# Kernel tuning notes

Measured on AMD Instinct MI355X. Metric: run time of the kernel, lower is better.

## Reference

```python
import jax, jax.numpy as jnp
import numpy as np

B, S, D, H, E, K = 16, 2048, 768, 3072, 8, 2
CAP_FACTOR = 1.25
LN_EPS = 1e-5


def setup_inputs() -> dict:
    key = jax.random.key(0)
    ks = jax.random.split(key, 6)
    scale = 0.02
    return {
        "x": jax.random.normal(ks[0], (B, S, D), jnp.float32),
        "w_gate": jax.random.normal(ks[1], (D, E), jnp.float32) * scale,  # router (eval: no noise)
        "w1": jax.random.normal(ks[2], (E, D, H), jnp.float32) * scale,
        "b1": jnp.zeros((E, H), jnp.float32),
        "w2": jax.random.normal(ks[3], (E, H, D), jnp.float32) * scale,
        "b2": jnp.zeros((E, D), jnp.float32),
        "ln_w": jnp.ones((D,), jnp.float32),
        "ln_b": jnp.zeros((D,), jnp.float32),
    }


def reference(x, w_gate, w1, b1, w2, b2, ln_w, ln_b):
    b, s, d = x.shape
    n = b * s
    capacity = int(CAP_FACTOR * n * K / E)  # static, matches _compute_capacity
    xf = x.reshape(n, d)

    # NoisyTopKRouter in eval mode: linear gate -> top-k -> softmax over top-k logits
    logits = xf @ w_gate                                   # [N, E]
    top_logits, top_idx = jax.lax.top_k(logits, K)         # [N, K]
    routing = jax.nn.softmax(top_logits, axis=-1)          # [N, K]

    out = jnp.zeros((n, d), x.dtype)
    for e in range(E):
        # per-token weight for expert e (0 if not routed to e)
        w_e = jnp.sum(routing * (top_idx == e), axis=-1)   # [N]
        # capacity dropping: keep the `capacity` highest-weight tokens.
        # Unassigned tokens have weight 0 -> zero contribution, so selecting
        # them as filler is mathematically identical to the torch loop.
        top_w, tok = jax.lax.top_k(w_e, capacity)          # [cap], [cap]
        sel = xf[tok]                                      # gather [cap, D]
        h = jax.nn.gelu(sel @ w1[e] + b1[e], approximate=False)
        y = h @ w2[e] + b2[e]                              # [cap, D]
        out = out.at[tok].add(y * top_w[:, None])          # weighted scatter-add

    out = out.reshape(b, s, d)
    mu = jnp.mean(out, axis=-1, keepdims=True)
    var = jnp.mean(jnp.square(out - mu), axis=-1, keepdims=True)
    return (out - mu) * jax.lax.rsqrt(var + LN_EPS) * ln_w + ln_b
```

## Files before the change

### kernel.cpp

```cpp
#include <hip/hip_runtime.h>
#include <math.h>

#define NTOK 32768
#define DDIM 768
#define HDIM 3072
#define NEXP 8
#define CAP  10240

typedef short short8 __attribute__((ext_vector_type(8)));
typedef float f32x4 __attribute__((ext_vector_type(4)));

__device__ __forceinline__ unsigned short f2bf(float f) {
  unsigned u = __float_as_uint(f);
  u += 0x7FFFu + ((u >> 16) & 1u);
  return (unsigned short)(u >> 16);
}
__device__ __forceinline__ float bf2f(unsigned short h) {
  return __uint_as_float((unsigned)h << 16);
}

__device__ __forceinline__ void gload16(const void* g, void* l) {
  __builtin_amdgcn_global_load_lds(
      (const __attribute__((address_space(1))) void*)g,
      (__attribute__((address_space(3))) void*)l, 16, 0, 0);
}

__device__ __forceinline__ float gelu_fast(float v) {
  float z = v * 0.70710678118654752f;
  float a = fabsf(z);
  float t = 1.0f / (1.0f + 0.3275911f * a);
  float p = t * (0.254829592f +
           t * (-0.284496736f +
           t * (1.421413741f +
           t * (-1.453152027f +
           t * 1.061405429f))));
  float ex = __expf(-a * a);
  float er = 1.0f - p * ex;
  er = copysignf(er, z);
  return 0.5f * v * (1.0f + er);
}

__global__ __launch_bounds__(256) void router_assign(
    const float* __restrict__ x, const float* __restrict__ wg,
    unsigned short* __restrict__ xb,
    unsigned int* __restrict__ pair, float* __restrict__ pw)
{
  __shared__ float wt[NEXP][DDIM];
  int t = threadIdx.x;
  for (int idx = t; idx < NEXP * DDIM; idx += 256) {
    int d = idx >> 3, e = idx & 7;
    wt[e][d] = wg[idx];
  }
  __syncthreads();
  int wave = t >> 6, lane = t & 63;
  int n0 = blockIdx.x * 32 + wave * 8;
  for (int i = 0; i < 8; ++i) {
    int n = n0 + i;
    const float* xr = x + (size_t)n * DDIM;
    unsigned short* xbr = xb + (size_t)n * DDIM;
    float acc[NEXP];
#pragma unroll
    for (int e = 0; e < NEXP; ++e) acc[e] = 0.f;
#pragma unroll
    for (int c = 0; c < 3; ++c) {
      int d = c * 256 + lane * 4;
      float4 xv = *(const float4*)(xr + d);
      ushort4 pk;
      pk.x = f2bf(xv.x); pk.y = f2bf(xv.y); pk.z = f2bf(xv.z); pk.w = f2bf(xv.w);
      *(ushort4*)(xbr + d) = pk;
#pragma unroll
      for (int e = 0; e < NEXP; ++e) {
        float4 wv = *(const float4*)(&wt[e][d]);
        acc[e] += xv.x * wv.x + xv.y * wv.y + xv.z * wv.z + xv.w * wv.w;
      }
    }
#pragma unroll
    for (int e = 0; e < NEXP; ++e) {
      float v = acc[e];
      for (int o = 32; o > 0; o >>= 1) v += __shfl_xor(v, o, 64);
      acc[e] = v;
    }
    if (lane == 0) {
      int e1 = 0; float l1 = acc[0];
#pragma unroll
      for (int e = 1; e < NEXP; ++e) if (acc[e] > l1) { l1 = acc[e]; e1 = e; }
      int e2 = -1; float l2 = -INFINITY;
#pragma unroll
      for (int e = 0; e < NEXP; ++e) if (e != e1 && acc[e] > l2) { l2 = acc[e]; e2 = e; }
      float p1 = 1.f / (1.f + expf(l2 - l1));
      pair[n] = (unsigned)e1 | ((unsigned)e2 << 8);
      pw[n] = p1;
    }
  }
}

__global__ __launch_bounds__(256) void router_scatter(
    const unsigned int* __restrict__ pair, int* __restrict__ cnt,
    int* __restrict__ tokidx, int* __restrict__ slotof)
{
  int e = blockIdx.x;
  __shared__ int wsum[4];
  __shared__ int basev;
  int t = threadIdx.x, wave = t >> 6, lane = t & 63;
  if (t == 0) basev = 0;
  __syncthreads();
  for (int nb = 0; nb < NTOK; nb += 256) {
    int n = nb + t;
    unsigned p = pair[n];
    int e1 = p & 255, e2 = (p >> 8) & 255;
    bool m2 = (e2 == e);
    bool m = (e1 == e) | m2;
    unsigned long long bal = __ballot(m);
    int pre = __popcll(bal & ((1ull << lane) - 1ull));
    if (lane == 0) wsum[wave] = __popcll(bal);
    __syncthreads();
    int woff = 0;
    for (int wv = 0; wv < wave; ++wv) woff += wsum[wv];
    int tot = wsum[0] + wsum[1] + wsum[2] + wsum[3];
    int pos = basev + woff + pre;
    if (m) {
      if (pos < CAP) {
        tokidx[e * CAP + pos] = n;
        slotof[2 * n + (m2 ? 1 : 0)] = e * CAP + pos;
      } else {
        slotof[2 * n + (m2 ? 1 : 0)] = -1;
      }
    }
    __syncthreads();
    if (t == 0) basev += tot;
  }
  __syncthreads();
  if (t == 0) cnt[e] = (basev < CAP) ? basev : CAP;
}

__global__ __launch_bounds__(256) void transpose_kernel(
    const float* __restrict__ src, unsigned short* __restrict__ dst, int R, int C)
{
  __shared__ float tile[64][65];
  int eb = blockIdx.z;
  const float* s = src + (size_t)eb * R * C;
  unsigned short* d = dst + (size_t)eb * R * C;
  int c0 = blockIdx.x * 64, r0 = blockIdx.y * 64;
  int tc = threadIdx.x & 63, tg = threadIdx.x >> 6;
#pragma unroll
  for (int rr = tg; rr < 64; rr += 4)
    tile[rr][tc] = s[(size_t)(r0 + rr) * C + c0 + tc];
  __syncthreads();
#pragma unroll
  for (int rr = tg; rr < 64; rr += 4)
    d[(size_t)(c0 + rr) * R + r0 + tc] = f2bf(tile[tc][rr]);
}

template<int EPI, int KK, int NN>
__global__ __launch_bounds__(512, 2) void moe_gemm(
    const unsigned short* __restrict__ A,
    const unsigned short* __restrict__ Bt,
    const float* __restrict__ bias,
    const int* __restrict__ cnt,
    const int* __restrict__ tokidx,
    unsigned short* __restrict__ Obuf,
    int mbase, int Mc, int mt)
{
  constexpr int KT = KK / 64;
  constexpr int NI = KT / 2;
  constexpr int GX = NN / 256;

  int nwg = gridDim.x;
  int orig = blockIdx.x;
  int q = nwg >> 3, r = nwg & 7;
  int xcd = orig & 7, loc = orig >> 3;
  int base = (xcd < r) ? xcd * (q + 1) : r * (q + 1) + (xcd - r) * q;
  int wg = base + loc;
  int per_e = GX * mt;
  int e = wg / per_e;
  int rem = wg - e * per_e;
  int by = rem / GX;
  int bx = rem - by * GX;

  int M = cnt[e]; if (M > CAP) M = CAP;
  int ly0 = by * 256;
  int gm0 = mbase + ly0;
  if (gm0 >= M) return;
  int n0 = bx * 256;
  int t = threadIdx.x, wave = t >> 6, lane = t & 63;
  int wr = wave >> 2, wc = wave & 3;
  int lane15 = lane & 15, quad = lane >> 4;

  __shared__ __align__(16) char smem[131072];

  int ci0 = wave * 128 + lane;
  int ci1 = ci0 + 64;
  int r0 = ci0 >> 2, r1 = ci1 >> 2;
  int c0 = (ci0 & 3) ^ ((r0 >> 1) & 3);
  int c1 = (ci1 & 3) ^ ((r1 >> 1) & 3);
  const unsigned short *aB0, *aB1, *bB0, *bB1;
  if (EPI == 0) {
    int g0 = gm0 + r0; if (g0 >= M) g0 = M - 1;
    int g1 = gm0 + r1; if (g1 >= M) g1 = M - 1;
    aB0 = A + (size_t)tokidx[e * CAP + g0] * KK + c0 * 8;
    aB1 = A + (size_t)tokidx[e * CAP + g1] * KK + c1 * 8;
  } else {
    aB0 = A + ((size_t)e * Mc + ly0 + r0) * KK + c0 * 8;
    aB1 = A + ((size_t)e * Mc + ly0 + r1) * KK + c1 * 8;
  }
  bB0 = Bt + ((size_t)e * NN + n0 + r0) * KK + c0 * 8;
  bB1 = Bt + ((size_t)e * NN + n0 + r1) * KK + c1 * 8;

#define STAGE_A(buf, kh, kt_) do { \
    gload16(aB0 + (kt_) * 64 + (kh) * 32, smem + (buf) * 65536 + (kh) * 16384 + wave * 2048); \
    gload16(aB1 + (kt_) * 64 + (kh) * 32, smem + (buf) * 65536 + (kh) * 16384 + wave * 2048 + 1024); \
  } while (0)
#define STAGE_B(buf, kh, kt_) do { \
    gload16(bB0 + (kt_) * 64 + (kh) * 32, smem + (buf) * 65536 + 32768 + (kh) * 16384 + wave * 2048); \
    gload16(bB1 + (kt_) * 64 + (kh) * 32, smem + (buf) * 65536 + 32768 + (kh) * 16384 + wave * 2048 + 1024); \
  } while (0)

  int aoffb[8], boffb[4];
#pragma unroll
  for (int m = 0; m < 8; ++m) {
    int row = wr * 128 + m * 16 + lane15;
    aoffb[m] = row * 64 + ((quad ^ ((row >> 1) & 3)) * 16);
  }
#pragma unroll
  for (int n = 0; n < 4; ++n) {
    int row = wc * 64 + n * 16 + lane15;
    boffb[n] = 32768 + row * 64 + ((quad ^ ((row >> 1) & 3)) * 16);
  }

  f32x4 acc[8][4];
#pragma unroll
  for (int mf = 0; mf < 8; ++mf)
#pragma unroll
    for (int n = 0; n < 4; ++n)
#pragma unroll
      for (int r = 0; r < 4; ++r) acc[mf][n][r] = 0.f;

  short8 af[4], bf[4];

#define BAR()  __builtin_amdgcn_s_barrier()
#define WVM8() asm volatile("s_waitcnt vmcnt(8)" ::: "memory")
#define WVM4() asm volatile("s_waitcnt vmcnt(4)" ::: "memory")
#define WVM0() asm volatile("s_waitcnt vmcnt(0)" ::: "memory")
#define RD_B(buf, ks) do { \
    _Pragma("unroll") \
    for (int n = 0; n < 4; ++n) \
      bf[n] = *(const short8*)(smem + (buf) * 65536 + (ks) * 16384 + boffb[n]); \
  } while (0)
#define RD_A(buf, ks, mh) do { \
    _Pragma("unroll") \
    for (int m = 0; m < 4; ++m) \
      af[m] = *(const short8*)(smem + (buf) * 65536 + (ks) * 16384 + aoffb[(mh) * 4 + m]); \
  } while (0)
#define MM(mh) do { \
    __builtin_amdgcn_s_setprio(1); \
    _Pragma("unroll") \
    for (int m = 0; m < 4; ++m) \
      _Pragma("unroll") \
      for (int n = 0; n < 4; ++n) \
        acc[(mh) * 4 + m][n] = __builtin_amdgcn_mfma_f32_16x16x32_bf16( \
            af[m], bf[n], acc[(mh) * 4 + m][n], 0, 0, 0); \
    __builtin_amdgcn_s_setprio(0); \
  } while (0)

  STAGE_A(0, 0, 0); STAGE_B(0, 0, 0);
  STAGE_A(0, 1, 0); STAGE_B(0, 1, 0);
  STAGE_A(1, 0, 1); STAGE_B(1, 0, 1);
  WVM8();
  BAR();

#pragma unroll 1
  for (int it = 0; it < NI - 1; ++it) {
    int kt = 2 * it;
    RD_B(0, 0); RD_A(0, 0, 0); STAGE_A(1, 1, kt + 1);
    BAR(); MM(0); BAR();
    RD_A(0, 0, 1); STAGE_B(1, 1, kt + 1);
    BAR(); MM(1); WVM8(); BAR();
    RD_B(0, 1); RD_A(0, 1, 0); STAGE_A(0, 0, kt + 2);
    BAR(); MM(0); BAR();
    RD_A(0, 1, 1); STAGE_B(0, 0, kt + 2);
    BAR(); MM(1); WVM8(); BAR();
    RD_B(1, 0); RD_A(1, 0, 0); STAGE_A(0, 1, kt + 2);
    BAR(); MM(0); BAR();
    RD_A(1, 0, 1); STAGE_B(0, 1, kt + 2);
    BAR(); MM(1); WVM8(); BAR();
    RD_B(1, 1); RD_A(1, 1, 0); STAGE_A(1, 0, kt + 3);
    BAR(); MM(0); BAR();
    RD_A(1, 1, 1); STAGE_B(1, 0, kt + 3);
    BAR(); MM(1); WVM8(); BAR();
  }

  {
    constexpr int kt = 2 * (NI - 1);
    RD_B(0, 0); RD_A(0, 0, 0); STAGE_A(1, 1, kt + 1);
    BAR(); MM(0); BAR();
    RD_A(0, 0, 1); STAGE_B(1, 1, kt + 1);
    BAR(); MM(1); WVM8(); BAR();
    RD_B(0, 1); RD_A(0, 1, 0);
    BAR(); MM(0); BAR();
    RD_A(0, 1, 1);
    BAR(); MM(1); WVM4(); BAR();
    RD_B(1, 0); RD_A(1, 0, 0);
    BAR(); MM(0); BAR();
    RD_A(1, 0, 1);
    BAR(); MM(1); WVM0(); BAR();
    RD_B(1, 1); RD_A(1, 1, 0);
    BAR(); MM(0); BAR();
    RD_A(1, 1, 1);
    BAR(); MM(1);
  }

  if (EPI == 0) {
#pragma unroll
    for (int n = 0; n < 4; ++n) {
      int col = n0 + wc * 64 + n * 16 + lane15;
      float bcol = bias[e * NN + col];
#pragma unroll
      for (int mf = 0; mf < 8; ++mf) {
        int rowb = ly0 + wr * 128 + mf * 16 + quad * 4;
#pragma unroll
        for (int r = 0; r < 4; ++r) {
          float v = gelu_fast(acc[mf][n][r] + bcol);
          Obuf[((size_t)e * Mc + rowb + r) * NN + col] = f2bf(v);
        }
      }
    }
  } else {
    float bc[4];
#pragma unroll
    for (int n = 0; n < 4; ++n)
      bc[n] = bias[e * NN + n0 + wc * 64 + n * 16 + lane15];
#pragma unroll
    for (int mf = 0; mf < 8; ++mf) {
      int gmb = gm0 + wr * 128 + mf * 16 + quad * 4;
#pragma unroll
      for (int r = 0; r < 4; ++r) {
        int gm = gmb + r;
        if (gm < M) {
          unsigned short* yrow = Obuf + ((size_t)e * CAP + gm) * NN;
#pragma unroll
          for (int n = 0; n < 4; ++n) {
            int col = n0 + wc * 64 + n * 16 + lane15;
            yrow[col] = f2bf(acc[mf][n][r] + bc[n]);
          }
        }
      }
    }
  }
#undef STAGE_A
#undef STAGE_B
#undef BAR
#undef WVM8
#undef WVM4
#undef WVM0
#undef RD_B
#undef RD_A
#undef MM
}

__global__ __launch_bounds__(256) void combine_ln(
    const unsigned short* __restrict__ Y, const int* __restrict__ slotof,
    const float* __restrict__ pw,
    const float* __restrict__ lnw, const float* __restrict__ lnb,
    float* __restrict__ out)
{
  __shared__ float red[8];
  int n = blockIdx.x;
  int s0 = slotof[2 * n], s1 = slotof[2 * n + 1];
  float p0 = pw[n], p1 = 1.f - p0;
  const unsigned short* y0 = Y + (size_t)(s0 < 0 ? 0 : s0) * DDIM;
  const unsigned short* y1 = Y + (size_t)(s1 < 0 ? 0 : s1) * DDIM;
  if (s0 < 0) p0 = 0.f;
  if (s1 < 0) p1 = 0.f;
  int t = threadIdx.x;
  float v0 = p0 * bf2f(y0[t])       + p1 * bf2f(y1[t]);
  float v1 = p0 * bf2f(y0[t + 256]) + p1 * bf2f(y1[t + 256]);
  float v2 = p0 * bf2f(y0[t + 512]) + p1 * bf2f(y1[t + 512]);
  float s = v0 + v1 + v2;
  float ss = v0 * v0 + v1 * v1 + v2 * v2;
  for (int o = 32; o > 0; o >>= 1) { s += __shfl_xor(s, o, 64); ss += __shfl_xor(ss, o, 64); }
  int wave = t >> 6, lane = t & 63;
  if (lane == 0) { red[wave] = s; red[4 + wave] = ss; }
  __syncthreads();
  s = red[0] + red[1] + red[2] + red[3];
  ss = red[4] + red[5] + red[6] + red[7];
  float mu = s * (1.f / DDIM);
  float var = ss * (1.f / DDIM) - mu * mu;
  float rs = rsqrtf(var + 1e-5f);
  float* row = out + (size_t)n * DDIM;
  row[t]       = (v0 - mu) * rs * lnw[t]       + lnb[t];
  row[t + 256] = (v1 - mu) * rs * lnw[t + 256] + lnb[t + 256];
  row[t + 512] = (v2 - mu) * rs * lnw[t + 512] + lnb[t + 512];
}

__global__ void sentinel_kernel(float* __restrict__ out, int n) {
  int i = blockIdx.x * 256 + threadIdx.x;
  if (i < n) out[i] = 12345.0f;
}

extern "C" void kernel_launch(void* const* d_in, const int* in_sizes, int n_in,
                              void* d_out, int out_size, void* d_ws, size_t ws_size,
                              hipStream_t stream)
{
  const float* x   = (const float*)d_in[0];
  const float* wg  = (const float*)d_in[1];
  const float* w1  = (const float*)d_in[2];
  const float* b1  = (const float*)d_in[3];
  const float* w2  = (const float*)d_in[4];
  const float* b2  = (const float*)d_in[5];
  const float* lnw = (const float*)d_in[6];
  const float* lnb = (const float*)d_in[7];
  float* out = (float*)d_out;

  char* ws = (char*)d_ws;
  size_t off = 0;
  auto take = [&](size_t bytes) {
    char* p = ws + off; off += (bytes + 255) & ~(size_t)255; return p;
  };
  unsigned short* xb   = (unsigned short*)take((size_t)NTOK * DDIM * 2);
  unsigned short* w1bt = (unsigned short*)take((size_t)NEXP * DDIM * HDIM * 2);
  unsigned short* w2bt = (unsigned short*)take((size_t)NEXP * DDIM * HDIM * 2);
  int*   tokidx = (int*)take((size_t)NEXP * CAP * 4);
  unsigned int* pair = (unsigned int*)take((size_t)NTOK * 4);
  float* pw   = (float*)take((size_t)NTOK * 4);
  int*   slotof = (int*)take((size_t)NTOK * 2 * 4);
  int*   cnt  = (int*)take(256);
  unsigned short* Ybuf = (unsigned short*)take((size_t)NEXP * CAP * DDIM * 2);

  size_t avail = (ws_size > off) ? (ws_size - off) : 0;
  long long cand = (long long)(avail / ((size_t)NEXP * HDIM * 2));
  int Mc = (int)((cand / 256) * 256);
  if (Mc > CAP) Mc = CAP;
  if (Mc < 256) {
    sentinel_kernel<<<(NTOK * DDIM + 255) / 256, 256, 0, stream>>>(out, NTOK * DDIM);
    return;
  }
  unsigned short* Hbuf = (unsigned short*)take((size_t)NEXP * Mc * HDIM * 2);

  router_assign<<<NTOK / 32, 256, 0, stream>>>(x, wg, xb, pair, pw);
  transpose_kernel<<<dim3(HDIM / 64, DDIM / 64, NEXP), 256, 0, stream>>>(w1, w1bt, DDIM, HDIM);
  transpose_kernel<<<dim3(DDIM / 64, HDIM / 64, NEXP), 256, 0, stream>>>(w2, w2bt, HDIM, DDIM);
  router_scatter<<<NEXP, 256, 0, stream>>>(pair, cnt, tokidx, slotof);

  for (int mbase = 0; mbase < CAP; mbase += Mc) {
    int rows = CAP - mbase; if (rows > Mc) rows = Mc;
    int mt = rows / 256;
    moe_gemm<0, DDIM, HDIM><<<(HDIM / 256) * mt * NEXP, 512, 0, stream>>>(
        xb, w1bt, b1, cnt, tokidx, Hbuf, mbase, Mc, mt);
    moe_gemm<1, HDIM, DDIM><<<(DDIM / 256) * mt * NEXP, 512, 0, stream>>>(
        Hbuf, w2bt, b2, cnt, tokidx, Ybuf, mbase, Mc, mt);
  }

  combine_ln<<<NTOK, 256, 0, stream>>>(Ybuf, slotof, pw, lnw, lnb, out);
}
```

Baseline: 1.514 ms.

## Parallelize token routing scatter, merge weight transposes, wave-per-token combine LN

```diff
diff --git a/kernel.cpp b/kernel.cpp
--- a/kernel.cpp
+++ b/kernel.cpp
@@ -6,6 +6,7 @@
 #define HDIM 3072
 #define NEXP 8
 #define CAP  10240
+#define NBLK 128
 
 typedef short short8 __attribute__((ext_vector_type(8)));
 typedef float f32x4 __attribute__((ext_vector_type(4)));
@@ -94,61 +95,95 @@
   }
 }
 
-__global__ __launch_bounds__(256) void router_scatter(
-    const unsigned int* __restrict__ pair, int* __restrict__ cnt,
+__global__ __launch_bounds__(256) void moe_count(
+    const unsigned int* __restrict__ pair, int* __restrict__ bcnt)
+{
+  __shared__ int c8[NEXP];
+  int b = blockIdx.x, t = threadIdx.x, lane = t & 63;
+  if (t < NEXP) c8[t] = 0;
+  __syncthreads();
+  unsigned p = pair[b * 256 + t];
+  int e1 = p & 255, e2 = (p >> 8) & 255;
+#pragma unroll
+  for (int e = 0; e < NEXP; ++e) {
+    int c = __popcll(__ballot(e1 == e)) + __popcll(__ballot(e2 == e));
+    if (lane == 0 && c) atomicAdd(&c8[e], c);
+  }
+  __syncthreads();
+  if (t < NEXP) bcnt[b * NEXP + t] = c8[t];
+}
+
+__global__ __launch_bounds__(512) void moe_scan(
+    const int* __restrict__ bcnt, int* __restrict__ bbase, int* __restrict__ cnt)
+{
+  int t = threadIdx.x, w = t >> 6, lane = t & 63;
+  if (lane == 0) {
+    int run = 0;
+    for (int b = 0; b < NBLK; ++b) { bbase[b * NEXP + w] = run; run += bcnt[b * NEXP + w]; }
+    cnt[w] = (run < CAP) ? run : CAP;
+  }
+}
+
+__global__ __launch_bounds__(256) void moe_scatter(
+    const unsigned int* __restrict__ pair, const int* __restrict__ bbase,
     int* __restrict__ tokidx, int* __restrict__ slotof)
 {
-  int e = blockIdx.x;
-  __shared__ int wsum[4];
-  __shared__ int basev;
-  int t = threadIdx.x, wave = t >> 6, lane = t & 63;
-  if (t == 0) basev = 0;
+  __shared__ int wcnt[4][NEXP];
+  __shared__ int woffs[4][NEXP];
+  int b = blockIdx.x, t = threadIdx.x, wave = t >> 6, lane = t & 63;
+  int n = b * 256 + t;
+  unsigned p = pair[n];
+  int e1 = p & 255, e2 = (p >> 8) & 255;
+  unsigned long long below = (lane == 63) ? 0x7FFFFFFFFFFFFFFFull
+                                          : ((1ull << lane) - 1ull);
+  int pre1 = 0, pre2 = 0;
+#pragma unroll
+  for (int e = 0; e < NEXP; ++e) {
+    unsigned long long b1 = __ballot(e1 == e);
+    unsigned long long b2 = __ballot(e2 == e);
+    if (e1 == e) pre1 = __popcll(b1 & below);
+    if (e2 == e) pre2 = __popcll(b1) + __popcll(b2 & below);
+    if (lane == 0) wcnt[wave][e] = __popcll(b1) + __popcll(b2);
+  }
   __syncthreads();
-  for (int nb = 0; nb < NTOK; nb += 256) {
-    int n = nb + t;
-    unsigned p = pair[n];
-    int e1 = p & 255, e2 = (p >> 8) & 255;
-    bool m2 = (e2 == e);
-    bool m = (e1 == e) | m2;
-    unsigned long long bal = __ballot(m);
-    int pre = __popcll(bal & ((1ull << lane) - 1ull));
-    if (lane == 0) wsum[wave] = __popcll(bal);
-    __syncthreads();
-    int woff = 0;
-    for (int wv = 0; wv < wave; ++wv) woff += wsum[wv];
-    int tot = wsum[0] + wsum[1] + wsum[2] + wsum[3];
-    int pos = basev + woff + pre;
-    if (m) {
-      if (pos < CAP) {
-        tokidx[e * CAP + pos] = n;
-        slotof[2 * n + (m2 ? 1 : 0)] = e * CAP + pos;
-      } else {
-        slotof[2 * n + (m2 ? 1 : 0)] = -1;
-      }
-    }
-    __syncthreads();
-    if (t == 0) basev += tot;
+  if (t < 4 * NEXP) {
+    int w = t >> 3, e = t & 7;
+    int s = 0;
+    for (int w2 = 0; w2 < w; ++w2) s += wcnt[w2][e];
+    woffs[w][e] = s;
   }
   __syncthreads();
-  if (t == 0) cnt[e] = (basev < CAP) ? basev : CAP;
-}
-
-__global__ __launch_bounds__(256) void transpose_kernel(
-    const float* __restrict__ src, unsigned short* __restrict__ dst, int R, int C)
+  int g1 = bbase[b * NEXP + e1] + woffs[wave][e1] + pre1;
+  int g2 = bbase[b * NEXP + e2] + woffs[wave][e2] + pre2;
+  if (g1 < CAP) { tokidx[e1 * CAP + g1] = n; slotof[2 * n] = e1 * CAP + g1; }
+  else slotof[2 * n] = -1;
+  if (g2 < CAP) { tokidx[e2 * CAP + g2] = n; slotof[2 * n + 1] = e2 * CAP + g2; }
+  else slotof[2 * n + 1] = -1;
+}
+
+__global__ __launch_bounds__(256) void transpose_all(
+    const float* __restrict__ w1, const float* __restrict__ w2,
+    unsigned short* __restrict__ d1, unsigned short* __restrict__ d2)
 {
   __shared__ float tile[64][65];
-  int eb = blockIdx.z;
-  const float* s = src + (size_t)eb * R * C;
-  unsigned short* d = dst + (size_t)eb * R * C;
-  int c0 = blockIdx.x * 64, r0 = blockIdx.y * 64;
+  int bid = blockIdx.x;
+  int half = bid / (576 * NEXP);
+  int r = bid - half * 576 * NEXP;
+  int e = r / 576, rr = r - e * 576;
+  const float* src; unsigned short* dst; int R, C, cx, cy;
+  if (half == 0) { src = w1; dst = d1; R = DDIM; C = HDIM; cx = rr % 48; cy = rr / 48; }
+  else           { src = w2; dst = d2; R = HDIM; C = DDIM; cx = rr % 12; cy = rr / 12; }
+  const float* s = src + (size_t)e * R * C;
+  unsigned short* d = dst + (size_t)e * R * C;
+  int c0 = cx * 64, r0 = cy * 64;
   int tc = threadIdx.x & 63, tg = threadIdx.x >> 6;
 #pragma unroll
-  for (int rr = tg; rr < 64; rr += 4)
-    tile[rr][tc] = s[(size_t)(r0 + rr) * C + c0 + tc];
+  for (int q = tg; q < 64; q += 4)
+    tile[q][tc] = s[(size_t)(r0 + q) * C + c0 + tc];
   __syncthreads();
 #pragma unroll
-  for (int rr = tg; rr < 64; rr += 4)
-    d[(size_t)(c0 + rr) * R + r0 + tc] = f2bf(tile[tc][rr]);
+  for (int q = tg; q < 64; q += 4)
+    d[(size_t)(c0 + q) * R + r0 + tc] = f2bf(tile[tc][q]);
 }
 
 template<int EPI, int KK, int NN>
@@ -233,7 +268,7 @@
 #pragma unroll
     for (int n = 0; n < 4; ++n)
 #pragma unroll
-      for (int r = 0; r < 4; ++r) acc[mf][n][r] = 0.f;
+      for (int r2 = 0; r2 < 4; ++r2) acc[mf][n][r2] = 0.f;
 
   short8 af[4], bf[4];
 
@@ -318,9 +353,9 @@
       for (int mf = 0; mf < 8; ++mf) {
         int rowb = ly0 + wr * 128 + mf * 16 + quad * 4;
 #pragma unroll
-        for (int r = 0; r < 4; ++r) {
-          float v = gelu_fast(acc[mf][n][r] + bcol);
-          Obuf[((size_t)e * Mc + rowb + r) * NN + col] = f2bf(v);
+        for (int r2 = 0; r2 < 4; ++r2) {
+          float v = gelu_fast(acc[mf][n][r2] + bcol);
+          Obuf[((size_t)e * Mc + rowb + r2) * NN + col] = f2bf(v);
         }
       }
     }
@@ -333,14 +368,14 @@
     for (int mf = 0; mf < 8; ++mf) {
       int gmb = gm0 + wr * 128 + mf * 16 + quad * 4;
 #pragma unroll
-      for (int r = 0; r < 4; ++r) {
-        int gm = gmb + r;
+      for (int r2 = 0; r2 < 4; ++r2) {
+        int gm = gmb + r2;
         if (gm < M) {
           unsigned short* yrow = Obuf + ((size_t)e * CAP + gm) * NN;
 #pragma unroll
           for (int n = 0; n < 4; ++n) {
             int col = n0 + wc * 64 + n * 16 + lane15;
-            yrow[col] = f2bf(acc[mf][n][r] + bc[n]);
+            yrow[col] = f2bf(acc[mf][n][r2] + bc[n]);
           }
         }
       }
@@ -357,39 +392,53 @@
 #undef MM
 }
 
-__global__ __launch_bounds__(256) void combine_ln(
+__global__ __launch_bounds__(512) void combine_ln(
     const unsigned short* __restrict__ Y, const int* __restrict__ slotof,
     const float* __restrict__ pw,
     const float* __restrict__ lnw, const float* __restrict__ lnb,
     float* __restrict__ out)
 {
-  __shared__ float red[8];
-  int n = blockIdx.x;
+  int w = threadIdx.x >> 6, lane = threadIdx.x & 63;
+  int n = blockIdx.x * 8 + w;
   int s0 = slotof[2 * n], s1 = slotof[2 * n + 1];
   float p0 = pw[n], p1 = 1.f - p0;
   const unsigned short* y0 = Y + (size_t)(s0 < 0 ? 0 : s0) * DDIM;
   const unsigned short* y1 = Y + (size_t)(s1 < 0 ? 0 : s1) * DDIM;
   if (s0 < 0) p0 = 0.f;
   if (s1 < 0) p1 = 0.f;
-  int t = threadIdx.x;
-  float v0 = p0 * bf2f(y0[t])       + p1 * bf2f(y1[t]);
-  float v1 = p0 * bf2f(y0[t + 256]) + p1 * bf2f(y1[t + 256]);
-  float v2 = p0 * bf2f(y0[t + 512]) + p1 * bf2f(y1[t + 512]);
-  float s = v0 + v1 + v2;
-  float ss = v0 * v0 + v1 * v1 + v2 * v2;
+  float v[12];
+  float s = 0.f, ss = 0.f;
+#pragma unroll
+  for (int c = 0; c < 3; ++c) {
+    int d = c * 256 + lane * 4;
+    ushort4 a = *(const ushort4*)(y0 + d);
+    ushort4 b = *(const ushort4*)(y1 + d);
+    float4 fa = { bf2f(a.x), bf2f(a.y), bf2f(a.z), bf2f(a.w) };
+    float4 fb = { bf2f(b.x), bf2f(b.y), bf2f(b.z), bf2f(b.w) };
+    v[c * 4 + 0] = p0 * fa.x + p1 * fb.x;
+    v[c * 4 + 1] = p0 * fa.y + p1 * fb.y;
+    v[c * 4 + 2] = p0 * fa.z + p1 * fb.z;
+    v[c * 4 + 3] = p0 * fa.w + p1 * fb.w;
+#pragma unroll
+    for (int j = 0; j < 4; ++j) { s += v[c * 4 + j]; ss += v[c * 4 + j] * v[c * 4 + j]; }
+  }
   for (int o = 32; o > 0; o >>= 1) { s += __shfl_xor(s, o, 64); ss += __shfl_xor(ss, o, 64); }
-  int wave = t >> 6, lane = t & 63;
-  if (lane == 0) { red[wave] = s; red[4 + wave] = ss; }
-  __syncthreads();
-  s = red[0] + red[1] + red[2] + red[3];
-  ss = red[4] + red[5] + red[6] + red[7];
   float mu = s * (1.f / DDIM);
   float var = ss * (1.f / DDIM) - mu * mu;
   float rs = rsqrtf(var + 1e-5f);
   float* row = out + (size_t)n * DDIM;
-  row[t]       = (v0 - mu) * rs * lnw[t]       + lnb[t];
-  row[t + 256] = (v1 - mu) * rs * lnw[t + 256] + lnb[t + 256];
-  row[t + 512] = (v2 - mu) * rs * lnw[t + 512] + lnb[t + 512];
+#pragma unroll
+  for (int c = 0; c < 3; ++c) {
+    int d = c * 256 + lane * 4;
+    float4 lw = *(const float4*)(lnw + d);
+    float4 lb = *(const float4*)(lnb + d);
+    float4 o;
+    o.x = (v[c * 4 + 0] - mu) * rs * lw.x + lb.x;
+    o.y = (v[c * 4 + 1] - mu) * rs * lw.y + lb.y;
+    o.z = (v[c * 4 + 2] - mu) * rs * lw.z + lb.z;
+    o.w = (v[c * 4 + 3] - mu) * rs * lw.w + lb.w;
+    *(float4*)(row + d) = o;
+  }
 }
 
 __global__ void sentinel_kernel(float* __restrict__ out, int n) {
@@ -424,6 +473,8 @@
   float* pw   = (float*)take((size_t)NTOK * 4);
   int*   slotof = (int*)take((size_t)NTOK * 2 * 4);
   int*   cnt  = (int*)take(256);
+  int*   bcnt  = (int*)take((size_t)NBLK * NEXP * 4);
+  int*   bbase = (int*)take((size_t)NBLK * NEXP * 4);
   unsigned short* Ybuf = (unsigned short*)take((size_t)NEXP * CAP * DDIM * 2);
 
   size_t avail = (ws_size > off) ? (ws_size - off) : 0;
@@ -437,9 +488,10 @@
   unsigned short* Hbuf = (unsigned short*)take((size_t)NEXP * Mc * HDIM * 2);
 
   router_assign<<<NTOK / 32, 256, 0, stream>>>(x, wg, xb, pair, pw);
-  transpose_kernel<<<dim3(HDIM / 64, DDIM / 64, NEXP), 256, 0, stream>>>(w1, w1bt, DDIM, HDIM);
-  transpose_kernel<<<dim3(DDIM / 64, HDIM / 64, NEXP), 256, 0, stream>>>(w2, w2bt, HDIM, DDIM);
-  router_scatter<<<NEXP, 256, 0, stream>>>(pair, cnt, tokidx, slotof);
+  transpose_all<<<576 * NEXP * 2, 256, 0, stream>>>(w1, w2, w1bt, w2bt);
+  moe_count<<<NBLK, 256, 0, stream>>>(pair, bcnt);
+  moe_scan<<<1, 512, 0, stream>>>(bcnt, bbase, cnt);
+  moe_scatter<<<NBLK, 256, 0, stream>>>(pair, bbase, tokidx, slotof);
 
   for (int mbase = 0; mbase < CAP; mbase += Mc) {
     int rows = CAP - mbase; if (rows > Mc) rows = Mc;
@@ -450,5 +502,5 @@
         Hbuf, w2bt, b2, cnt, tokidx, Ybuf, mbase, Mc, mt);
   }
 
-  combine_ln<<<NTOK, 256, 0, stream>>>(Ybuf, slotof, pw, lnw, lnb, out);
-}
+  combine_ln<<<NTOK / 8, 512, 0, stream>>>(Ybuf, slotof, pw, lnw, lnb, out);
+}
```

Result: faster. 1.450 ms (-4.2%).
